# Optimization experiments

Hardware: AMD Instinct MI355X
Metric: run time of the kernel (lower is better)

## Reference

```python
import jax, jax.numpy as jnp
import numpy as np

EMBED_DIM = 1024
N = 8192


def setup_inputs() -> dict:
    key = jax.random.key(0)
    k1, k2, k3 = jax.random.split(key, 3)
    inputs = jax.random.normal(k1, (N, EMBED_DIM), dtype=jnp.float32)
    rotation = jax.random.normal(k2, (EMBED_DIM, EMBED_DIM), dtype=jnp.float32)
    entangle = jax.random.normal(k3, (EMBED_DIM, EMBED_DIM), dtype=jnp.float32)
    return {"inputs": inputs, "rotation": rotation, "entangle": entangle}


def reference(inputs, rotation, entangle):
    # inputs: [N, D]; rotation/entangle: [D, D]
    query = inputs @ rotation          # [N, D]
    key = inputs @ entangle            # [N, D]
    scale = 1.0 / np.sqrt(inputs.shape[-1]).astype(np.float32)
    logits = (query @ key.T) * scale   # [N, N]
    scores = jax.nn.softmax(logits, axis=-1)
    return scores @ inputs             # [N, D]
```

## Files before the change

### kernel.cpp

```cpp
#include <hip/hip_runtime.h>


typedef _Float16 f16;
typedef _Float16 f16x4 __attribute__((ext_vector_type(4)));
typedef _Float16 f16x8 __attribute__((ext_vector_type(8)));
typedef float    f32x4 __attribute__((ext_vector_type(4)));
typedef unsigned int u32;

#define N_ROWS 8192
#define D_DIM  1024
#define LOG2E  1.44269504088896340736f

__device__ __forceinline__ void gload_lds16(const void* g, void* l) {
  __builtin_amdgcn_global_load_lds(
      (const __attribute__((address_space(1))) u32*)g,
      (__attribute__((address_space(3))) u32*)l, 16, 0, 0);
}

__device__ __forceinline__ f16x8 read_frag(const f16* tile, int row, int lane) {
  int kb = ((lane >> 4) & 3) << 4;
  int phys = row * 64 + (kb ^ (((row >> 1) & 3) << 4));
  return *(const f16x8*)((const char*)tile + phys);
}

__device__ __forceinline__ f16x8 read_frag64(const f16* tile, int row, int lane, int ks2) {
  int kb = ks2 * 64 + (((lane >> 4) & 3) << 4);
  int phys = row * 128 + (kb ^ ((row & 7) << 4));
  return *(const f16x8*)((const char*)tile + phys);
}

__global__ __launch_bounds__(256) void splitk(const float* __restrict__ in,
                                              f16* __restrict__ hi, f16* __restrict__ lo,
                                              int n4) {
  int i = blockIdx.x * 256 + threadIdx.x;
  if (i >= n4) return;
  float4 v = ((const float4*)in)[i];
  float vv[4] = {v.x, v.y, v.z, v.w};
  f16x4 h, l;
#pragma unroll
  for (int j = 0; j < 4; ++j) {
    f16 hh = (f16)vv[j];
    h[j] = hh;
    l[j] = (f16)(vv[j] - (float)hh);
  }
  *(f16x4*)(hi + (size_t)i * 4) = h;
  *(f16x4*)(lo + (size_t)i * 4) = l;
}

__global__ __launch_bounds__(256) void transpose_cast(const float* __restrict__ X,
                                                      f16* __restrict__ Xt) {
  __shared__ float tile[32][33];
  int bx = blockIdx.x, by = blockIdx.y;
  int tx = threadIdx.x & 31, ty0 = threadIdx.x >> 5;
#pragma unroll
  for (int r = 0; r < 4; ++r) {
    int ty = ty0 + r * 8;
    tile[ty][tx] = X[(size_t)(by * 32 + ty) * D_DIM + bx * 32 + tx];
  }
  __syncthreads();
#pragma unroll
  for (int r = 0; r < 4; ++r) {
    int ty = ty0 + r * 8;
    Xt[(size_t)(bx * 32 + ty) * N_ROWS + by * 32 + tx] = (f16)tile[tx][ty];
  }
}

template <int OUT_SPLIT>
__global__ __launch_bounds__(256) void gemm_abt(
    const f16* __restrict__ Ahi, const f16* __restrict__ Alo,
    const f16* __restrict__ Bhi, const f16* __restrict__ Blo,
    float scale, int Ncols,
    float* __restrict__ C, f16* __restrict__ Chi, f16* __restrict__ Clo) {
  __shared__ __align__(16) f16 lds[4 * 4096];
  const int t = threadIdx.x, w = t >> 6, l = t & 63;
  const int bn = blockIdx.x, bm = blockIdx.y;
  const int wr = (w >> 1) * 64, wc = (w & 1) * 64;
  const char* srcs[4];
  srcs[0] = (const char*)(Ahi + (size_t)bm * 128 * 1024);
  srcs[1] = (const char*)(Alo + (size_t)bm * 128 * 1024);
  srcs[2] = (const char*)(Bhi + (size_t)bn * 128 * 1024);
  srcs[3] = (const char*)(Blo + (size_t)bn * 128 * 1024);
  f32x4 acc[4][4] = {};
  for (int ks = 0; ks < 32; ++ks) {
#pragma unroll
    for (int tt = 0; tt < 4; ++tt)
#pragma unroll
      for (int j = 0; j < 2; ++j) {
        int seg = j * 4 + w;
        int p = seg * 1024 + l * 16;
        int r = p >> 6;
        int sw = (p & 63) ^ (((r >> 1) & 3) << 4);
        gload_lds16(srcs[tt] + (size_t)r * 2048 + ks * 64 + sw,
                    (char*)lds + tt * 8192 + seg * 1024);
      }
    __syncthreads();
    f16x8 ah[4], al[4], bh[4], bl[4];
#pragma unroll
    for (int m = 0; m < 4; ++m) {
      int row = wr + m * 16 + (l & 15);
      ah[m] = read_frag(lds, row, l);
      al[m] = read_frag(lds + 4096, row, l);
    }
#pragma unroll
    for (int n = 0; n < 4; ++n) {
      int row = wc + n * 16 + (l & 15);
      bh[n] = read_frag(lds + 8192, row, l);
      bl[n] = read_frag(lds + 12288, row, l);
    }
#pragma unroll
    for (int m = 0; m < 4; ++m)
#pragma unroll
      for (int n = 0; n < 4; ++n) {
        acc[m][n] = __builtin_amdgcn_mfma_f32_16x16x32_f16(ah[m], bh[n], acc[m][n], 0, 0, 0);
        acc[m][n] = __builtin_amdgcn_mfma_f32_16x16x32_f16(ah[m], bl[n], acc[m][n], 0, 0, 0);
        acc[m][n] = __builtin_amdgcn_mfma_f32_16x16x32_f16(al[m], bh[n], acc[m][n], 0, 0, 0);
      }
    __syncthreads();
  }
#pragma unroll
  for (int m = 0; m < 4; ++m)
#pragma unroll
    for (int n = 0; n < 4; ++n)
#pragma unroll
      for (int j = 0; j < 4; ++j) {
        int row = bm * 128 + wr + m * 16 + ((l >> 4) << 2) + j;
        int col = bn * 128 + wc + n * 16 + (l & 15);
        float v = acc[m][n][j] * scale;
        size_t idx = (size_t)row * Ncols + col;
        if (OUT_SPLIT) {
          f16 hh = (f16)v;
          Chi[idx] = hh;
          Clo[idx] = (f16)(v - (float)hh);
        } else {
          C[idx] = v;
        }
      }
}

__global__ __launch_bounds__(256) void pexp(const float* __restrict__ L,
                                            f16* __restrict__ P) {
  const int row = blockIdx.x, t = threadIdx.x, w = t >> 6, l = t & 63;
  const float4* p = (const float4*)(L + (size_t)row * N_ROWS);
  __shared__ float red[8];
  float4 v[8];
#pragma unroll
  for (int i = 0; i < 8; ++i) v[i] = p[t + i * 256];
  float mx = -3.4e38f;
#pragma unroll
  for (int i = 0; i < 8; ++i)
    mx = fmaxf(mx, fmaxf(fmaxf(v[i].x, v[i].y), fmaxf(v[i].z, v[i].w)));
#pragma unroll
  for (int off = 32; off; off >>= 1) mx = fmaxf(mx, __shfl_xor(mx, off));
  if (l == 0) red[w] = mx;
  __syncthreads();
  mx = fmaxf(fmaxf(red[0], red[1]), fmaxf(red[2], red[3]));
  float e[8][4];
  float s = 0.f;
#pragma unroll
  for (int i = 0; i < 8; ++i) {
    e[i][0] = exp2f((v[i].x - mx) * LOG2E);
    e[i][1] = exp2f((v[i].y - mx) * LOG2E);
    e[i][2] = exp2f((v[i].z - mx) * LOG2E);
    e[i][3] = exp2f((v[i].w - mx) * LOG2E);
    s += (e[i][0] + e[i][1]) + (e[i][2] + e[i][3]);
  }
#pragma unroll
  for (int off = 32; off; off >>= 1) s += __shfl_xor(s, off);
  if (l == 0) red[4 + w] = s;
  __syncthreads();
  float sinv = 1.0f / (red[4] + red[5] + red[6] + red[7]);
  f16* prow = P + (size_t)row * 16384;
#pragma unroll
  for (int i = 0; i < 8; ++i) {
    f16x4 h;
    h[0] = (f16)(e[i][0] * sinv);
    h[1] = (f16)(e[i][1] * sinv);
    h[2] = (f16)(e[i][2] * sinv);
    h[3] = (f16)(e[i][3] * sinv);
    *(f16x4*)(prow + (size_t)(t + i * 256) * 4) = h;
  }
}

__global__ __launch_bounds__(256) void gemm_pv(
    const f16* __restrict__ P,
    const f16* __restrict__ Xt,
    float* __restrict__ out) {
  __shared__ __align__(16) f16 ldsA[64 * 64];
  __shared__ __align__(16) f16 ldsB[128 * 64];
  const int t = threadIdx.x, w = t >> 6, l = t & 63;
  const int bn = blockIdx.x, bm = blockIdx.y;
  const int wr = (w >> 1) * 32, wc = (w & 1) * 64;
  const char* Abase = (const char*)(P + (size_t)bm * 64 * 16384);
  const char* Bbase = (const char*)(Xt + (size_t)bn * 128 * 8192);
  f32x4 acc[2][4] = {};
  for (int ks = 0; ks < 128; ++ks) {
#pragma unroll
    for (int s = 0; s < 2; ++s) {
      int p = s * 4096 + t * 16;
      int r = p >> 7, q = p & 127;
      int sq = q ^ ((r & 7) << 4);
      gload_lds16(Abase + (size_t)r * 32768 + ks * 128 + sq, (char*)ldsA + p);
    }
#pragma unroll
    for (int s = 0; s < 4; ++s) {
      int p = s * 4096 + t * 16;
      int r = p >> 7, q = p & 127;
      int sq = q ^ ((r & 7) << 4);
      gload_lds16(Bbase + (size_t)r * 16384 + ks * 128 + sq, (char*)ldsB + p);
    }
    __syncthreads();
#pragma unroll
    for (int ks2 = 0; ks2 < 2; ++ks2) {
      f16x8 a[2], b[4];
#pragma unroll
      for (int m = 0; m < 2; ++m) a[m] = read_frag64(ldsA, wr + m * 16 + (l & 15), l, ks2);
#pragma unroll
      for (int n = 0; n < 4; ++n) b[n] = read_frag64(ldsB, wc + n * 16 + (l & 15), l, ks2);
#pragma unroll
      for (int m = 0; m < 2; ++m)
#pragma unroll
        for (int n = 0; n < 4; ++n)
          acc[m][n] = __builtin_amdgcn_mfma_f32_16x16x32_f16(a[m], b[n], acc[m][n], 0, 0, 0);
    }
    __syncthreads();
  }
#pragma unroll
  for (int m = 0; m < 2; ++m)
#pragma unroll
    for (int n = 0; n < 4; ++n)
#pragma unroll
      for (int j = 0; j < 4; ++j) {
        int row = bm * 64 + wr + m * 16 + ((l >> 4) << 2) + j;
        int col = bn * 128 + wc + n * 16 + (l & 15);
        out[(size_t)row * D_DIM + col] = acc[m][n][j];
      }
}

extern "C" void kernel_launch(void* const* d_in, const int* in_sizes, int n_in,
                              void* d_out, int out_size, void* d_ws, size_t ws_size,
                              hipStream_t stream) {
  const float* X = (const float*)d_in[0];
  const float* R = (const float*)d_in[1];
  const float* E = (const float*)d_in[2];
  float* out = (float*)d_out;

  char* p = (char*)d_ws;
  auto alloc = [&](size_t bytes) -> char* {
    char* r = p;
    p += (bytes + 255) & ~(size_t)255;
    return r;
  };
  f16* Xhi = (f16*)alloc((size_t)N_ROWS * D_DIM * 2);
  f16* Xlo = (f16*)alloc((size_t)N_ROWS * D_DIM * 2);
  f16* Yhi = (f16*)alloc((size_t)N_ROWS * D_DIM * 2);
  f16* Ylo = (f16*)alloc((size_t)N_ROWS * D_DIM * 2);
  f16* Xt  = (f16*)alloc((size_t)N_ROWS * D_DIM * 2);
  float* Lbuf = (float*)p;
  size_t front = (size_t)(p - (char*)d_ws);

  char* tail = (char*)d_ws + ws_size;
  auto alloct = [&](size_t bytes) -> char* {
    tail = (char*)(((uintptr_t)tail - bytes) & ~(uintptr_t)255);
    return tail;
  };
  f16* Rhi  = (f16*)alloct((size_t)D_DIM * D_DIM * 2);
  f16* Rlo  = (f16*)alloct((size_t)D_DIM * D_DIM * 2);
  f16* Ehi  = (f16*)alloct((size_t)D_DIM * D_DIM * 2);
  f16* Elo  = (f16*)alloct((size_t)D_DIM * D_DIM * 2);
  f16* Mthi = (f16*)alloct((size_t)D_DIM * D_DIM * 2);
  f16* Mtlo = (f16*)alloct((size_t)D_DIM * D_DIM * 2);

  size_t avail = ws_size > front ? ws_size - front : 0;
  int CH = (int)(avail / ((size_t)N_ROWS * 4));
  if (CH > N_ROWS) CH = N_ROWS;
  CH &= ~127;
  if (CH < 128) CH = 128;

  splitk<<<dim3((N_ROWS * D_DIM / 4 + 255) / 256), 256, 0, stream>>>(X, Xhi, Xlo, N_ROWS * D_DIM / 4);
  splitk<<<dim3((D_DIM * D_DIM / 4 + 255) / 256), 256, 0, stream>>>(R, Rhi, Rlo, D_DIM * D_DIM / 4);
  splitk<<<dim3((D_DIM * D_DIM / 4 + 255) / 256), 256, 0, stream>>>(E, Ehi, Elo, D_DIM * D_DIM / 4);
  transpose_cast<<<dim3(D_DIM / 32, N_ROWS / 32), 256, 0, stream>>>(X, Xt);

  gemm_abt<1><<<dim3(8, 8), 256, 0, stream>>>(Ehi, Elo, Rhi, Rlo, 1.0f, D_DIM,
                                              nullptr, Mthi, Mtlo);
  gemm_abt<1><<<dim3(8, 64), 256, 0, stream>>>(Xhi, Xlo, Mthi, Mtlo, 1.0f, D_DIM,
                                               nullptr, Yhi, Ylo);

  for (int c0 = 0; c0 < N_ROWS; c0 += CH) {
    int rows = (N_ROWS - c0 < CH) ? (N_ROWS - c0) : CH;
    gemm_abt<0><<<dim3(N_ROWS / 128, rows / 128), 256, 0, stream>>>(
        Yhi + (size_t)c0 * D_DIM, Ylo + (size_t)c0 * D_DIM, Xhi, Xlo,
        0.03125f, N_ROWS, Lbuf, nullptr, nullptr);
    pexp<<<dim3(rows), 256, 0, stream>>>(Lbuf, (f16*)Lbuf);
    gemm_pv<<<dim3(D_DIM / 128, rows / 64), 256, 0, stream>>>(
        (const f16*)Lbuf, Xt, out + (size_t)c0 * D_DIM);
  }
}
```

Measured before the change: 868.6 us.

## Use 256x256 double-buffered tile kernel for the logits GEMM

Adds a dedicated kernel for the N x N logits GEMM that uses 512 threads, 256x256 output tiles and double-buffered LDS staging via global_load_lds, so the next k-tile is prefetched while MFMAs run on the current one. The larger tile raises arithmetic intensity per loaded byte, and the double buffer is meant to overlap loads with compute. The old templated kernel is kept only for the split-output projection GEMMs, and the chunk size is rounded to multiples of 256. The risks are the 128 KB LDS footprint and high register use (8x4 accumulators), which limit occupancy.

New measurement: 776.7 us. 10.6% less time.

```diff
diff --git a/kernel.cpp b/kernel.cpp
--- a/kernel.cpp
+++ b/kernel.cpp
@@ -65,12 +65,10 @@
   }
 }
 
-template <int OUT_SPLIT>
-__global__ __launch_bounds__(256) void gemm_abt(
+__global__ __launch_bounds__(256) void gemm_abt_s(
     const f16* __restrict__ Ahi, const f16* __restrict__ Alo,
     const f16* __restrict__ Bhi, const f16* __restrict__ Blo,
-    float scale, int Ncols,
-    float* __restrict__ C, f16* __restrict__ Chi, f16* __restrict__ Clo) {
+    int Ncols, f16* __restrict__ Chi, f16* __restrict__ Clo) {
   __shared__ __align__(16) f16 lds[4 * 4096];
   const int t = threadIdx.x, w = t >> 6, l = t & 63;
   const int bn = blockIdx.x, bm = blockIdx.y;
@@ -125,15 +123,80 @@
       for (int j = 0; j < 4; ++j) {
         int row = bm * 128 + wr + m * 16 + ((l >> 4) << 2) + j;
         int col = bn * 128 + wc + n * 16 + (l & 15);
-        float v = acc[m][n][j] * scale;
+        float v = acc[m][n][j];
         size_t idx = (size_t)row * Ncols + col;
-        if (OUT_SPLIT) {
-          f16 hh = (f16)v;
-          Chi[idx] = hh;
-          Clo[idx] = (f16)(v - (float)hh);
-        } else {
-          C[idx] = v;
-        }
+        f16 hh = (f16)v;
+        Chi[idx] = hh;
+        Clo[idx] = (f16)(v - (float)hh);
+      }
+}
+
+__global__ __launch_bounds__(512, 2) void gemm_abt_big(
+    const f16* __restrict__ Ahi, const f16* __restrict__ Alo,
+    const f16* __restrict__ Bhi, const f16* __restrict__ Blo,
+    float scale, float* __restrict__ C) {
+  __shared__ __align__(16) f16 lds[2][4 * 8192];
+  const int t = threadIdx.x, w = t >> 6, l = t & 63;
+  const int bn = blockIdx.x, bm = blockIdx.y;
+  const int wm = w >> 2, wn = w & 3;
+  const char* srcs[4];
+  srcs[0] = (const char*)(Ahi + (size_t)bm * 256 * 1024);
+  srcs[1] = (const char*)(Alo + (size_t)bm * 256 * 1024);
+  srcs[2] = (const char*)(Bhi + (size_t)bn * 256 * 1024);
+  srcs[3] = (const char*)(Blo + (size_t)bn * 256 * 1024);
+
+#define STAGE_BIG(buf, kt)                                                   \
+  {                                                                          \
+    _Pragma("unroll") for (int rnd = 0; rnd < 8; ++rnd) {                    \
+      int phys = rnd * 8192 + t * 16;           \
+      int tile = phys >> 14;                                                 \
+      int r = (phys & 16383) >> 6;                                           \
+      int q = phys & 63;                                                     \
+      int sw = q ^ (((r >> 1) & 3) << 4);                                    \
+      gload_lds16(srcs[tile] + (size_t)r * 2048 + (kt) * 64 + sw,            \
+                  (char*)&lds[buf][0] + phys);                               \
+    }                                                                        \
+  }
+
+  f32x4 acc[8][4] = {};
+  STAGE_BIG(0, 0);
+  __syncthreads();
+  int cur = 0;
+  for (int kt = 0; kt < 32; ++kt) {
+    if (kt < 31) STAGE_BIG(cur ^ 1, kt + 1);
+    const f16* Lb = &lds[cur][0];
+    f16x8 bh[4], bl[4];
+#pragma unroll
+    for (int n = 0; n < 4; ++n) {
+      int row = wn * 64 + n * 16 + (l & 15);
+      bh[n] = read_frag(Lb + 16384, row, l);
+      bl[n] = read_frag(Lb + 24576, row, l);
+    }
+#pragma unroll
+    for (int m = 0; m < 8; ++m) {
+      int row = wm * 128 + m * 16 + (l & 15);
+      f16x8 ah = read_frag(Lb, row, l);
+      f16x8 al = read_frag(Lb + 8192, row, l);
+#pragma unroll
+      for (int n = 0; n < 4; ++n) {
+        acc[m][n] = __builtin_amdgcn_mfma_f32_16x16x32_f16(ah, bh[n], acc[m][n], 0, 0, 0);
+        acc[m][n] = __builtin_amdgcn_mfma_f32_16x16x32_f16(ah, bl[n], acc[m][n], 0, 0, 0);
+        acc[m][n] = __builtin_amdgcn_mfma_f32_16x16x32_f16(al, bh[n], acc[m][n], 0, 0, 0);
+      }
+    }
+    __syncthreads();
+    cur ^= 1;
+  }
+#undef STAGE_BIG
+#pragma unroll
+  for (int m = 0; m < 8; ++m)
+#pragma unroll
+    for (int n = 0; n < 4; ++n)
+#pragma unroll
+      for (int j = 0; j < 4; ++j) {
+        int row = bm * 256 + wm * 128 + m * 16 + ((l >> 4) << 2) + j;
+        int col = bn * 256 + wn * 64 + n * 16 + (l & 15);
+        C[(size_t)row * N_ROWS + col] = acc[m][n][j] * scale;
       }
 }
 
@@ -273,24 +336,22 @@
   size_t avail = ws_size > front ? ws_size - front : 0;
   int CH = (int)(avail / ((size_t)N_ROWS * 4));
   if (CH > N_ROWS) CH = N_ROWS;
-  CH &= ~127;
-  if (CH < 128) CH = 128;
+  CH &= ~255;
+  if (CH < 256) CH = 256;
 
   splitk<<<dim3((N_ROWS * D_DIM / 4 + 255) / 256), 256, 0, stream>>>(X, Xhi, Xlo, N_ROWS * D_DIM / 4);
   splitk<<<dim3((D_DIM * D_DIM / 4 + 255) / 256), 256, 0, stream>>>(R, Rhi, Rlo, D_DIM * D_DIM / 4);
   splitk<<<dim3((D_DIM * D_DIM / 4 + 255) / 256), 256, 0, stream>>>(E, Ehi, Elo, D_DIM * D_DIM / 4);
   transpose_cast<<<dim3(D_DIM / 32, N_ROWS / 32), 256, 0, stream>>>(X, Xt);
 
-  gemm_abt<1><<<dim3(8, 8), 256, 0, stream>>>(Ehi, Elo, Rhi, Rlo, 1.0f, D_DIM,
-                                              nullptr, Mthi, Mtlo);
-  gemm_abt<1><<<dim3(8, 64), 256, 0, stream>>>(Xhi, Xlo, Mthi, Mtlo, 1.0f, D_DIM,
-                                               nullptr, Yhi, Ylo);
+  gemm_abt_s<<<dim3(8, 8), 256, 0, stream>>>(Ehi, Elo, Rhi, Rlo, D_DIM, Mthi, Mtlo);
+  gemm_abt_s<<<dim3(8, 64), 256, 0, stream>>>(Xhi, Xlo, Mthi, Mtlo, D_DIM, Yhi, Ylo);
 
   for (int c0 = 0; c0 < N_ROWS; c0 += CH) {
     int rows = (N_ROWS - c0 < CH) ? (N_ROWS - c0) : CH;
-    gemm_abt<0><<<dim3(N_ROWS / 128, rows / 128), 256, 0, stream>>>(
+    gemm_abt_big<<<dim3(N_ROWS / 256, rows / 256), 512, 0, stream>>>(
         Yhi + (size_t)c0 * D_DIM, Ylo + (size_t)c0 * D_DIM, Xhi, Xlo,
-        0.03125f, N_ROWS, Lbuf, nullptr, nullptr);
+        0.03125f, Lbuf);
     pexp<<<dim3(rows), 256, 0, stream>>>(Lbuf, (f16*)Lbuf);
     gemm_pv<<<dim3(D_DIM / 128, rows / 64), 256, 0, stream>>>(
         (const f16*)Lbuf, Xt, out + (size_t)c0 * D_DIM);
```
